# Optimization experiments

Measured on AMD Instinct MI355X. Metric: run time of the kernel, lower is better.

## Reference

```python
import jax, jax.numpy as jnp
import numpy as np

BATCH, OUT_FEATURES = 512, 1024
NUM_BLOCKS, LATTICE_DIM = 32, 4
MAX_INDICES = 256  # q^lattice_dim with q=4, lattice_dim=4


def setup_inputs() -> dict:
    key = jax.random.key(0)
    k1, k2, k3 = jax.random.split(key, 3)
    input_indices = jax.random.randint(k1, (BATCH, NUM_BLOCKS, LATTICE_DIM), 0, MAX_INDICES, dtype=jnp.int64 if jax.config.jax_enable_x64 else jnp.int32)
    weight_indices = jax.random.randint(k2, (OUT_FEATURES, NUM_BLOCKS, LATTICE_DIM), 0, MAX_INDICES, dtype=jnp.int64 if jax.config.jax_enable_x64 else jnp.int32)
    lut_table = jax.random.normal(k3, (MAX_INDICES, MAX_INDICES), dtype=jnp.float32)
    return {"input_indices": input_indices, "weight_indices": weight_indices, "lut_table": lut_table}


def reference(input_indices, weight_indices, lut_table):
    # Flatten block/lattice dims: K = num_blocks * lattice_dim
    B = input_indices.shape[0]
    O = weight_indices.shape[0]
    inp = jnp.clip(input_indices.reshape(B, -1), 0, MAX_INDICES - 1)   # [B, K]
    wgt = jnp.clip(weight_indices.reshape(O, -1), 0, MAX_INDICES - 1)  # [O, K]
    # out[b, o] = sum_k LUT[inp[b, k], wgt[o, k]]
    vals = lut_table[inp[:, None, :], wgt[None, :, :]]  # [B, O, K] gather
    return jnp.sum(vals, axis=-1)  # [B, O]
```

## Files before the change

### kernel.cpp

```cpp
#include <hip/hip_runtime.h>


#define BATCH 512
#define OUTF  1024
#define KDIM  128
#define MIDX  256

typedef _Float16 half4v __attribute__((ext_vector_type(4)));

__global__ __launch_bounds__(1024, 1)
void slt_kernel(const int* __restrict__ inp, const int* __restrict__ wgt,
                const float* __restrict__ lut, float* __restrict__ out) {
    __shared__ __attribute__((aligned(16))) _Float16 lut16[MIDX * MIDX];
    __shared__ __attribute__((aligned(16))) unsigned int wrow_pack[16 * 32];
    __shared__ __attribute__((aligned(16))) unsigned int wcol_pack[8 * 128 * 4];

    const int tid   = threadIdx.x;
    const int otile = blockIdx.x;
    const int btile = blockIdx.y;

    const float4* lut4 = (const float4*)lut;
    half4v* l16v = (half4v*)lut16;
    #pragma unroll
    for (int it = 0; it < 16; ++it) {
        int idx = it * 1024 + tid;
        float4 v = lut4[idx];
        half4v h = { (_Float16)v.x, (_Float16)v.y, (_Float16)v.z, (_Float16)v.w };
        l16v[idx] = h;
    }

    if (tid < 512) {
        int b = tid >> 5;
        int q = tid & 31;
        const int4 iv = *(const int4*)(inp + ((size_t)(btile * 16 + b)) * KDIM + q * 4);
        wrow_pack[b * 32 + q] = (unsigned int)(iv.x & 255)
                              | ((unsigned int)(iv.y & 255) << 8)
                              | ((unsigned int)(iv.z & 255) << 16)
                              | ((unsigned int)(iv.w & 255) << 24);
    }

    {
        int o = tid >> 3;
        int jj = tid & 7;
        const int* wbase = wgt + ((size_t)(otile * 128 + o)) * KDIM;
        #pragma unroll
        for (int i = 0; i < 4; ++i) {
            int q = jj + 8 * i;
            const int4 wv = *(const int4*)(wbase + q * 4);
            unsigned int pw = (unsigned int)(wv.x & 255)
                            | ((unsigned int)(wv.y & 255) << 8)
                            | ((unsigned int)(wv.z & 255) << 16)
                            | ((unsigned int)(wv.w & 255) << 24);
            wcol_pack[(q >> 2) * 512 + o * 4 + (q & 3)] = pw;
        }
    }

    __syncthreads();

    const int w    = tid >> 6;
    const int lane = tid & 63;

    float a0 = 0.f, a1 = 0.f, b0 = 0.f, b1 = 0.f;

    #pragma unroll 2
    for (int g = 0; g < 8; ++g) {
        uint4 rw = *(const uint4*)&wrow_pack[w * 32 + 4 * g];
        uint4 c0 = *(const uint4*)&wcol_pack[g * 512 + lane * 4];
        uint4 c1 = *(const uint4*)&wcol_pack[g * 512 + (lane + 64) * 4];

        unsigned int rws[4] = { rw.x, rw.y, rw.z, rw.w };
        unsigned int w0s[4] = { c0.x, c0.y, c0.z, c0.w };
        unsigned int w1s[4] = { c1.x, c1.y, c1.z, c1.w };

        #pragma unroll
        for (int j = 0; j < 4; ++j) {
            unsigned int rword = (unsigned int)__builtin_amdgcn_readfirstlane((int)rws[j]);
            int rb0 = (int)((rword       & 255u) << 8);
            int rb1 = (int)(((rword >> 8) & 255u) << 8);
            int rb2 = (int)(((rword >> 16) & 255u) << 8);
            int rb3 = (int)((rword >> 24) << 8);
            unsigned int u0 = w0s[j], u1 = w1s[j];

            a0 += (float)lut16[rb0 + (int)(u0 & 255u)];
            a1 += (float)lut16[rb0 + (int)(u1 & 255u)];
            b0 += (float)lut16[rb1 + (int)((u0 >> 8) & 255u)];
            b1 += (float)lut16[rb1 + (int)((u1 >> 8) & 255u)];
            a0 += (float)lut16[rb2 + (int)((u0 >> 16) & 255u)];
            a1 += (float)lut16[rb2 + (int)((u1 >> 16) & 255u)];
            b0 += (float)lut16[rb3 + (int)(u0 >> 24)];
            b1 += (float)lut16[rb3 + (int)(u1 >> 24)];
        }
    }

    size_t ob = ((size_t)(btile * 16 + w)) * OUTF + (size_t)(otile * 128) + lane;
    out[ob]      = a0 + b0;
    out[ob + 64] = a1 + b1;
}

extern "C" void kernel_launch(void* const* d_in, const int* in_sizes, int n_in,
                              void* d_out, int out_size, void* d_ws, size_t ws_size,
                              hipStream_t stream) {
    const int*   inp = (const int*)d_in[0];
    const int*   wgt = (const int*)d_in[1];
    const float* lut = (const float*)d_in[2];
    float*       out = (float*)d_out;

    dim3 grid(8, 32);
    dim3 block(1024);
    slt_kernel<<<grid, block, 0, stream>>>(inp, wgt, lut, out);
}
```

Before: 73.54 us.

## Serve low LUT rows from a global fp16 copy to split gathers across LDS and cache

Each block now also writes the first 64 fp16-converted LUT rows to a global workspace. Lookups whose input index is below 64 gather from that global copy, and the rest keep using LDS, so that the LDS gather bandwidth is shared with the vector L1 cache. Input row indices are read per wave straight from global memory through a wave-uniform pointer instead of being packed into shared memory, and the &255 clamp on input indices is dropped. This risks the higher latency of global gathers and relies on every block redundantly writing the same workspace values.

```diff
diff --git a/kernel.cpp b/kernel.cpp
--- a/kernel.cpp
+++ b/kernel.cpp
@@ -1,7 +1,6 @@
 #include <hip/hip_runtime.h>
 
 
-#define BATCH 512
 #define OUTF  1024
 #define KDIM  128
 #define MIDX  256
@@ -10,9 +9,9 @@
 
 __global__ __launch_bounds__(1024, 1)
 void slt_kernel(const int* __restrict__ inp, const int* __restrict__ wgt,
-                const float* __restrict__ lut, float* __restrict__ out) {
+                const float* __restrict__ lut, float* __restrict__ out,
+                _Float16* __restrict__ wst) {
     __shared__ __attribute__((aligned(16))) _Float16 lut16[MIDX * MIDX];
-    __shared__ __attribute__((aligned(16))) unsigned int wrow_pack[16 * 32];
     __shared__ __attribute__((aligned(16))) unsigned int wcol_pack[8 * 128 * 4];
 
     const int tid   = threadIdx.x;
@@ -21,26 +20,18 @@
 
     const float4* lut4 = (const float4*)lut;
     half4v* l16v = (half4v*)lut16;
+    half4v* wsv  = (half4v*)wst;
     #pragma unroll
     for (int it = 0; it < 16; ++it) {
         int idx = it * 1024 + tid;
         float4 v = lut4[idx];
         half4v h = { (_Float16)v.x, (_Float16)v.y, (_Float16)v.z, (_Float16)v.w };
         l16v[idx] = h;
-    }
-
-    if (tid < 512) {
-        int b = tid >> 5;
-        int q = tid & 31;
-        const int4 iv = *(const int4*)(inp + ((size_t)(btile * 16 + b)) * KDIM + q * 4);
-        wrow_pack[b * 32 + q] = (unsigned int)(iv.x & 255)
-                              | ((unsigned int)(iv.y & 255) << 8)
-                              | ((unsigned int)(iv.z & 255) << 16)
-                              | ((unsigned int)(iv.w & 255) << 24);
+        if (it < 4) wsv[idx] = h;
     }
 
     {
-        int o = tid >> 3;
+        int o  = tid >> 3;
         int jj = tid & 7;
         const int* wbase = wgt + ((size_t)(otile * 128 + o)) * KDIM;
         #pragma unroll
@@ -57,44 +48,44 @@
 
     __syncthreads();
 
-    const int w    = tid >> 6;
+    const int w    = __builtin_amdgcn_readfirstlane(tid >> 6);
     const int lane = tid & 63;
+    const int* rowp = inp + ((size_t)(btile * 16 + w)) * KDIM;
 
     float a0 = 0.f, a1 = 0.f, b0 = 0.f, b1 = 0.f;
+    float v0 = 0.f, v1 = 0.f;
 
     #pragma unroll 2
     for (int g = 0; g < 8; ++g) {
-        uint4 rw = *(const uint4*)&wrow_pack[w * 32 + 4 * g];
-        uint4 c0 = *(const uint4*)&wcol_pack[g * 512 + lane * 4];
-        uint4 c1 = *(const uint4*)&wcol_pack[g * 512 + (lane + 64) * 4];
-
-        unsigned int rws[4] = { rw.x, rw.y, rw.z, rw.w };
-        unsigned int w0s[4] = { c0.x, c0.y, c0.z, c0.w };
-        unsigned int w1s[4] = { c1.x, c1.y, c1.z, c1.w };
+        uint4 cw0 = *(const uint4*)&wcol_pack[g * 512 + lane * 4];
+        uint4 cw1 = *(const uint4*)&wcol_pack[g * 512 + (lane + 64) * 4];
+        unsigned int w0s[4] = { cw0.x, cw0.y, cw0.z, cw0.w };
+        unsigned int w1s[4] = { cw1.x, cw1.y, cw1.z, cw1.w };
 
         #pragma unroll
         for (int j = 0; j < 4; ++j) {
-            unsigned int rword = (unsigned int)__builtin_amdgcn_readfirstlane((int)rws[j]);
-            int rb0 = (int)((rword       & 255u) << 8);
-            int rb1 = (int)(((rword >> 8) & 255u) << 8);
-            int rb2 = (int)(((rword >> 16) & 255u) << 8);
-            int rb3 = (int)((rword >> 24) << 8);
             unsigned int u0 = w0s[j], u1 = w1s[j];
-
-            a0 += (float)lut16[rb0 + (int)(u0 & 255u)];
-            a1 += (float)lut16[rb0 + (int)(u1 & 255u)];
-            b0 += (float)lut16[rb1 + (int)((u0 >> 8) & 255u)];
-            b1 += (float)lut16[rb1 + (int)((u1 >> 8) & 255u)];
-            a0 += (float)lut16[rb2 + (int)((u0 >> 16) & 255u)];
-            a1 += (float)lut16[rb2 + (int)((u1 >> 16) & 255u)];
-            b0 += (float)lut16[rb3 + (int)(u0 >> 24)];
-            b1 += (float)lut16[rb3 + (int)(u1 >> 24)];
+            #pragma unroll
+            for (int m = 0; m < 4; ++m) {
+                int r   = rowp[g * 16 + j * 4 + m];
+                int cc0 = (int)((u0 >> (8 * m)) & 255u);
+                int cc1 = (int)((u1 >> (8 * m)) & 255u);
+                if (r < 64) {
+                    const _Float16* p = wst + (r << 8);
+                    v0 += (float)p[cc0];
+                    v1 += (float)p[cc1];
+                } else {
+                    const _Float16* p = lut16 + (r << 8);
+                    if (m & 1) { b0 += (float)p[cc0]; b1 += (float)p[cc1]; }
+                    else       { a0 += (float)p[cc0]; a1 += (float)p[cc1]; }
+                }
+            }
         }
     }
 
     size_t ob = ((size_t)(btile * 16 + w)) * OUTF + (size_t)(otile * 128) + lane;
-    out[ob]      = a0 + b0;
-    out[ob + 64] = a1 + b1;
+    out[ob]      = a0 + b0 + v0;
+    out[ob + 64] = a1 + b1 + v1;
 }
 
 extern "C" void kernel_launch(void* const* d_in, const int* in_sizes, int n_in,
@@ -104,8 +95,9 @@
     const int*   wgt = (const int*)d_in[1];
     const float* lut = (const float*)d_in[2];
     float*       out = (float*)d_out;
+    _Float16*    wst = (_Float16*)d_ws;
 
     dim3 grid(8, 32);
     dim3 block(1024);
-    slt_kernel<<<grid, block, 0, stream>>>(inp, wgt, lut, out);
+    slt_kernel<<<grid, block, 0, stream>>>(inp, wgt, lut, out, wst);
 }
```

New measurement: 78.94 us. 1.07x slower.
